# Kernel optimization log

Measured on AMD Instinct MI355X. Metric: run time of the kernel, lower is better.

The kernel has to match this reference:

```python
import jax, jax.numpy as jnp
import numpy as np

N_NODES = 100000
N_EDGES = 1600000
N_GRAPHS = 512
IN_CH = 128
HID_CH = 128   # 2 * out_channels
OUT_CH = 64


def gcn_conv(x, edge_index, W, b, num_nodes):
    """PyG GCNConv: x' = D^-1/2 (A+I) D^-1/2 (x W) + b (symmetric norm, self loops)."""
    h = x @ W  # [N, F_out]
    loops = jnp.arange(num_nodes, dtype=edge_index.dtype)
    src = jnp.concatenate([edge_index[0], loops])  # j (source)
    dst = jnp.concatenate([edge_index[1], loops])  # i (target)
    deg = jax.ops.segment_sum(jnp.ones_like(dst, dtype=h.dtype), dst,
                              num_segments=num_nodes)  # in-degree incl. self loop
    dinv = jnp.where(deg > 0, jax.lax.rsqrt(deg), 0.0)
    norm = dinv[src] * dinv[dst]  # [E+N]
    msgs = h[src] * norm[:, None]  # gather + scale, [E+N, F_out]
    out = jax.ops.segment_sum(msgs, dst, num_segments=num_nodes)
    return out + b


def global_mean_pool(x, batch, num_graphs):
    sums = jax.ops.segment_sum(x, batch, num_segments=num_graphs)
    cnts = jax.ops.segment_sum(jnp.ones((x.shape[0],), x.dtype), batch,
                               num_segments=num_graphs)
    return sums / jnp.maximum(cnts, 1.0)[:, None]


def setup_inputs() -> dict:
    key = jax.random.key(0)
    k = jax.random.split(key, 6)
    x = jax.random.normal(k[0], (N_NODES, IN_CH), dtype=jnp.float32)
    edge_index = jax.random.randint(k[1], (2, N_EDGES), 0, N_NODES, dtype=jnp.int64)
    batch = jnp.sort(jax.random.randint(k[2], (N_NODES,), 0, N_GRAPHS, dtype=jnp.int64))
    W1 = jax.random.normal(k[3], (IN_CH, HID_CH), dtype=jnp.float32) * (1.0 / np.sqrt(IN_CH))
    b1 = jnp.zeros((HID_CH,), dtype=jnp.float32)
    W2 = jax.random.normal(k[4], (HID_CH, OUT_CH), dtype=jnp.float32) * (1.0 / np.sqrt(HID_CH))
    b2 = jnp.zeros((OUT_CH,), dtype=jnp.float32)
    return {"x": x, "edge_index": edge_index, "batch": batch,
            "W1": W1, "b1": b1, "W2": W2, "b2": b2}


def reference(x, edge_index, batch, W1, b1, W2, b2):
    h = gcn_conv(x, edge_index, W1, b1, N_NODES)
    h = jax.nn.relu(h)
    h = gcn_conv(h, edge_index, W2, b2, N_NODES)
    return global_mean_pool(h, batch, N_GRAPHS)  # [num_graphs, out_channels]
```

## Files before the change

kernel.cpp:

```cpp
#include <hip/hip_runtime.h>
#include <hip/hip_fp16.h>

#define NN 100000
#define NE 1600000
#define NG 512
#define NBLK 391
#define CAP 4608
#define EPBS 4096
#define NCBS 391

typedef _Float16 half8 __attribute__((ext_vector_type(8)));
typedef _Float16 half4v __attribute__((ext_vector_type(4)));
typedef float floatx4 __attribute__((ext_vector_type(4)));
typedef float floatx2 __attribute__((ext_vector_type(2)));

__device__ inline unsigned char f32_to_fp8(float v) {
    return (unsigned char)(__builtin_amdgcn_cvt_pk_fp8_f32(v, v, 0, false) & 0xFF);
}
__device__ inline void fp8x8_acc(float* acc, uint2 u) {
    floatx2 a = __builtin_amdgcn_cvt_pk_f32_fp8(u.x, false);
    floatx2 b = __builtin_amdgcn_cvt_pk_f32_fp8(u.x, true);
    floatx2 c = __builtin_amdgcn_cvt_pk_f32_fp8(u.y, false);
    floatx2 d = __builtin_amdgcn_cvt_pk_f32_fp8(u.y, true);
    acc[0] += a[0]; acc[1] += a[1]; acc[2] += b[0]; acc[3] += b[1];
    acc[4] += c[0]; acc[5] += c[1]; acc[6] += d[0]; acc[7] += d[1];
}

__global__ void k_wtboth(const float* __restrict__ W1, const float* __restrict__ W2,
                         __half* __restrict__ Wt1, __half* __restrict__ Wt2,
                         int* __restrict__ gcur) {
    int idx = blockIdx.x * 256 + threadIdx.x;
    if (idx < 128 * 128) {
        int k = idx >> 7, n = idx & 127;
        Wt1[n * 128 + k] = __float2half(W1[idx]);
    } else {
        int j = idx - 128 * 128;
        if (j < 128 * 64) {
            int k = j / 64, n = j % 64;
            Wt2[n * 128 + k] = __float2half(W2[j]);
        }
    }
    if (idx < 512) gcur[idx] = idx * CAP;
}

__global__ __launch_bounds__(256) void k_csort(const int* __restrict__ src,
                                               const int* __restrict__ dst,
                                               int* __restrict__ gcur,
                                               unsigned* __restrict__ pairbuf) {
    __shared__ int hcnt[NBLK];
    __shared__ int lbase[NBLK];
    __shared__ int lcur[NBLK];
    __shared__ int gbase[NBLK];
    __shared__ int ss[512];
    __shared__ unsigned sorted[EPBS];
    __shared__ unsigned short bkt[EPBS];
    int t = threadIdx.x;
    int e0 = blockIdx.x * EPBS;
    int e1 = e0 + EPBS; if (e1 > NE) e1 = NE;
    int n = e1 - e0;

    for (int i = t; i < NBLK; i += 256) hcnt[i] = 0;
    __syncthreads();
    for (int i = e0 + t; i < e1; i += 256)
        atomicAdd(&hcnt[dst[i] >> 8], 1);
    __syncthreads();
    ss[t]       = (t < NBLK) ? hcnt[t] : 0;
    ss[t + 256] = (t + 256 < NBLK) ? hcnt[t + 256] : 0;
    __syncthreads();
    for (int d = 1; d < 512; d <<= 1) {
        int v1 = (t >= d) ? ss[t - d] : 0;
        int v2 = ss[t + 256 - d];
        __syncthreads();
        ss[t] += v1; ss[t + 256] += v2;
        __syncthreads();
    }
    for (int i = t; i < NBLK; i += 256) {
        int ex = ss[i] - hcnt[i];
        lbase[i] = ex;
        lcur[i] = ex;
        if (hcnt[i] > 0) gbase[i] = atomicAdd(&gcur[i], hcnt[i]);
    }
    __syncthreads();
    for (int i = e0 + t; i < e1; i += 256) {
        int d = dst[i];
        int b = d >> 8;
        int pos = atomicAdd(&lcur[b], 1);
        sorted[pos] = ((unsigned)(d & 255) << 24) | (unsigned)src[i];
        bkt[pos] = (unsigned short)b;
    }
    __syncthreads();
    for (int i = t; i < n; i += 256) {
        int b = bkt[i];
        pairbuf[gbase[b] + (i - lbase[b])] = sorted[i];
    }
}

__global__ __launch_bounds__(256) void k_offs_place(
    const unsigned* __restrict__ pairbuf, const int* __restrict__ gcur,
    int* __restrict__ offs, int* __restrict__ edeg,
    float* __restrict__ dinv, int* __restrict__ csr) {
    __shared__ int dcnt[256];
    __shared__ int p[256];
    __shared__ int lcur[256];
    int t = threadIdx.x;
    int b = blockIdx.x;
    int base = b * CAP;
    int cnt = gcur[b] - base;
    int node0 = b << 8;
    dcnt[t] = 0;
    __syncthreads();
    for (int i = t; i < cnt; i += 256)
        atomicAdd(&dcnt[pairbuf[base + i] >> 24], 1);
    __syncthreads();
    int v = dcnt[t];
    p[t] = v;
    __syncthreads();
    for (int d = 1; d < 256; d <<= 1) {
        int u = (t >= d) ? p[t - d] : 0;
        __syncthreads();
        p[t] += u;
        __syncthreads();
    }
    int ex = p[t] - v;
    lcur[t] = ex;
    int node = node0 + t;
    if (node < NN) {
        offs[node] = base + ex;
        edeg[node] = v;
        dinv[node] = rsqrtf((float)(v + 1));
    }
    __syncthreads();
    for (int i = t; i < cnt; i += 256) {
        unsigned e = pairbuf[base + i];
        int slot = atomicAdd(&lcur[e >> 24], 1);
        csr[base + slot] = (int)(e & 0xFFFFFFu);
    }
}

__global__ __launch_bounds__(256) void k_mm_mfma(const float* __restrict__ X,
                                                 const __half* __restrict__ Wt,
                                                 const float* __restrict__ dinv,
                                                 unsigned char* __restrict__ Out) {
    constexpr int PITCH = 136;
    constexpr int FOUT = 128;
    __shared__ _Float16 Xs[64 * PITCH];
    __shared__ _Float16 Ws[FOUT * PITCH];
    int t = threadIdx.x;
    int row0 = blockIdx.x * 64;

    for (int i = t; i < 64 * 32; i += 256) {
        int r = i >> 5, f4 = i & 31;
        int row = row0 + r;
        half4v h = {};
        if (row < NN) {
            float4 v = *(const float4*)(X + (size_t)row * 128 + f4 * 4);
            h[0] = (_Float16)v.x; h[1] = (_Float16)v.y;
            h[2] = (_Float16)v.z; h[3] = (_Float16)v.w;
        }
        *(half4v*)(Xs + r * PITCH + f4 * 4) = h;
    }
    for (int i = t; i < FOUT * 16; i += 256) {
        int n = i >> 4, kg = i & 15;
        *(half8*)(Ws + n * PITCH + kg * 8) = *(const half8*)(Wt + n * 128 + kg * 8);
    }
    __syncthreads();

    int wave = t >> 6, lane = t & 63;
    int m = lane & 15, quad = lane >> 4;
    int wrow = wave * 16;
    constexpr int NCT = FOUT / 16;
    floatx4 acc[NCT];
#pragma unroll
    for (int c = 0; c < NCT; ++c) acc[c] = (floatx4){0.f, 0.f, 0.f, 0.f};

#pragma unroll
    for (int kc = 0; kc < 4; ++kc) {
        half8 a = *(const half8*)(Xs + (wrow + m) * PITCH + kc * 32 + quad * 8);
#pragma unroll
        for (int c = 0; c < NCT; ++c) {
            half8 b = *(const half8*)(Ws + (c * 16 + m) * PITCH + kc * 32 + quad * 8);
            acc[c] = __builtin_amdgcn_mfma_f32_16x16x32_f16(a, b, acc[c], 0, 0, 0);
        }
    }

    float dv[4];
    int rowb = row0 + wrow + quad * 4;
#pragma unroll
    for (int r = 0; r < 4; ++r) dv[r] = (rowb + r < NN) ? dinv[rowb + r] : 0.f;
#pragma unroll
    for (int c = 0; c < NCT; ++c) {
#pragma unroll
        for (int r = 0; r < 4; ++r) {
            int row = rowb + r;
            if (row < NN)
                Out[(size_t)row * FOUT + c * 16 + m] = f32_to_fp8(acc[c][r] * dv[r]);
        }
    }
}

__global__ __launch_bounds__(256) void k_agg_mm(
    const unsigned char* __restrict__ G, const int* __restrict__ csr,
    const int* __restrict__ offs, const int* __restrict__ edeg,
    const float* __restrict__ dinv, const float* __restrict__ bias1,
    const __half* __restrict__ Wt2, unsigned char* __restrict__ G2) {
    constexpr int PITCH = 136;
    __shared__ _Float16 Brows[16 * PITCH];
    __shared__ _Float16 Ws[64 * PITCH];
    int t = threadIdx.x;
    for (int i = t; i < 64 * 16; i += 256) {
        int n = i >> 4, kg = i & 15;
        *(half8*)(Ws + n * PITCH + kg * 8) = *(const half8*)(Wt2 + n * 128 + kg * 8);
    }
    int wave = t >> 6, lane = t & 63;
    int sub = lane >> 4, fl = lane & 15;
    int ni = wave * 4 + sub;
    int node = blockIdx.x * 16 + ni;
    float acc[8];
#pragma unroll
    for (int j = 0; j < 8; ++j) acc[j] = 0.f;
    fp8x8_acc(acc, *(const uint2*)(G + (size_t)node * 128 + fl * 8));
    int e0 = offs[node], e1 = e0 + edeg[node];
    int e = e0;
    if (e + 8 <= e1) {
        int s0 = csr[e],     s1 = csr[e + 1], s2 = csr[e + 2], s3 = csr[e + 3];
        int s4 = csr[e + 4], s5 = csr[e + 5], s6 = csr[e + 6], s7 = csr[e + 7];
        for (; e + 8 <= e1; e += 8) {
            int p0 = csr[e + 8],  p1 = csr[e + 9],  p2 = csr[e + 10], p3 = csr[e + 11];
            int p4 = csr[e + 12], p5 = csr[e + 13], p6 = csr[e + 14], p7 = csr[e + 15];
            uint2 v0 = *(const uint2*)(G + (size_t)s0 * 128 + fl * 8);
            uint2 v1 = *(const uint2*)(G + (size_t)s1 * 128 + fl * 8);
            uint2 v2 = *(const uint2*)(G + (size_t)s2 * 128 + fl * 8);
            uint2 v3 = *(const uint2*)(G + (size_t)s3 * 128 + fl * 8);
            uint2 v4 = *(const uint2*)(G + (size_t)s4 * 128 + fl * 8);
            uint2 v5 = *(const uint2*)(G + (size_t)s5 * 128 + fl * 8);
            uint2 v6 = *(const uint2*)(G + (size_t)s6 * 128 + fl * 8);
            uint2 v7 = *(const uint2*)(G + (size_t)s7 * 128 + fl * 8);
            fp8x8_acc(acc, v0); fp8x8_acc(acc, v1); fp8x8_acc(acc, v2); fp8x8_acc(acc, v3);
            fp8x8_acc(acc, v4); fp8x8_acc(acc, v5); fp8x8_acc(acc, v6); fp8x8_acc(acc, v7);
            s0 = p0; s1 = p1; s2 = p2; s3 = p3;
            s4 = p4; s5 = p5; s6 = p6; s7 = p7;
        }
    }
    for (; e + 4 <= e1; e += 4) {
        int s0 = csr[e], s1 = csr[e + 1], s2 = csr[e + 2], s3 = csr[e + 3];
        uint2 v0 = *(const uint2*)(G + (size_t)s0 * 128 + fl * 8);
        uint2 v1 = *(const uint2*)(G + (size_t)s1 * 128 + fl * 8);
        uint2 v2 = *(const uint2*)(G + (size_t)s2 * 128 + fl * 8);
        uint2 v3 = *(const uint2*)(G + (size_t)s3 * 128 + fl * 8);
        fp8x8_acc(acc, v0); fp8x8_acc(acc, v1); fp8x8_acc(acc, v2); fp8x8_acc(acc, v3);
    }
    for (; e < e1; ++e)
        fp8x8_acc(acc, *(const uint2*)(G + (size_t)csr[e] * 128 + fl * 8));
    {
        float di = dinv[node];
        float4 b0 = *(const float4*)(bias1 + fl * 8);
        float4 b1 = *(const float4*)(bias1 + fl * 8 + 4);
        half8 h;
        h[0] = (_Float16)fmaxf(acc[0] * di + b0.x, 0.f);
        h[1] = (_Float16)fmaxf(acc[1] * di + b0.y, 0.f);
        h[2] = (_Float16)fmaxf(acc[2] * di + b0.z, 0.f);
        h[3] = (_Float16)fmaxf(acc[3] * di + b0.w, 0.f);
        h[4] = (_Float16)fmaxf(acc[4] * di + b1.x, 0.f);
        h[5] = (_Float16)fmaxf(acc[5] * di + b1.y, 0.f);
        h[6] = (_Float16)fmaxf(acc[6] * di + b1.z, 0.f);
        h[7] = (_Float16)fmaxf(acc[7] * di + b1.w, 0.f);
        *(half8*)(Brows + ni * PITCH + fl * 8) = h;
    }
    __syncthreads();
    int m = lane & 15, quad = lane >> 4;
    floatx4 c = (floatx4){0.f, 0.f, 0.f, 0.f};
#pragma unroll
    for (int kc = 0; kc < 4; ++kc) {
        half8 a = *(const half8*)(Brows + m * PITCH + kc * 32 + quad * 8);
        half8 b = *(const half8*)(Ws + (wave * 16 + m) * PITCH + kc * 32 + quad * 8);
        c = __builtin_amdgcn_mfma_f32_16x16x32_f16(a, b, c, 0, 0, 0);
    }
    int rowb = blockIdx.x * 16 + quad * 4;
#pragma unroll
    for (int r = 0; r < 4; ++r) {
        float dv = dinv[rowb + r];
        G2[(size_t)(rowb + r) * 64 + wave * 16 + m] = f32_to_fp8(c[r] * dv);
    }
}

__global__ __launch_bounds__(256) void k_agg_pool(
    const unsigned char* __restrict__ G, const int* __restrict__ csr,
    const int* __restrict__ offs, const int* __restrict__ edeg,
    const float* __restrict__ dinv, const int* __restrict__ batch,
    float* __restrict__ gsum) {
    __shared__ float bsum[4][64];
    int t = threadIdx.x;
    int wave = t >> 6, lane = t & 63;
    int sub = lane >> 3, fl = lane & 7;
    int n0 = blockIdx.x * 32;
    int nb = n0 + wave * 8;
    int node = nb + sub;
    float acc[8];
#pragma unroll
    for (int j = 0; j < 8; ++j) acc[j] = 0.f;
    fp8x8_acc(acc, *(const uint2*)(G + (size_t)node * 64 + fl * 8));
    int e0 = offs[node], e1 = e0 + edeg[node];
    int e = e0;
    if (e + 8 <= e1) {
        int s0 = csr[e],     s1 = csr[e + 1], s2 = csr[e + 2], s3 = csr[e + 3];
        int s4 = csr[e + 4], s5 = csr[e + 5], s6 = csr[e + 6], s7 = csr[e + 7];
        for (; e + 8 <= e1; e += 8) {
            int p0 = csr[e + 8],  p1 = csr[e + 9],  p2 = csr[e + 10], p3 = csr[e + 11];
            int p4 = csr[e + 12], p5 = csr[e + 13], p6 = csr[e + 14], p7 = csr[e + 15];
            uint2 v0 = *(const uint2*)(G + (size_t)s0 * 64 + fl * 8);
            uint2 v1 = *(const uint2*)(G + (size_t)s1 * 64 + fl * 8);
            uint2 v2 = *(const uint2*)(G + (size_t)s2 * 64 + fl * 8);
            uint2 v3 = *(const uint2*)(G + (size_t)s3 * 64 + fl * 8);
            uint2 v4 = *(const uint2*)(G + (size_t)s4 * 64 + fl * 8);
            uint2 v5 = *(const uint2*)(G + (size_t)s5 * 64 + fl * 8);
            uint2 v6 = *(const uint2*)(G + (size_t)s6 * 64 + fl * 8);
            uint2 v7 = *(const uint2*)(G + (size_t)s7 * 64 + fl * 8);
            fp8x8_acc(acc, v0); fp8x8_acc(acc, v1); fp8x8_acc(acc, v2); fp8x8_acc(acc, v3);
            fp8x8_acc(acc, v4); fp8x8_acc(acc, v5); fp8x8_acc(acc, v6); fp8x8_acc(acc, v7);
            s0 = p0; s1 = p1; s2 = p2; s3 = p3;
            s4 = p4; s5 = p5; s6 = p6; s7 = p7;
        }
    }
    for (; e + 4 <= e1; e += 4) {
        int s0 = csr[e], s1 = csr[e + 1], s2 = csr[e + 2], s3 = csr[e + 3];
        uint2 v0 = *(const uint2*)(G + (size_t)s0 * 64 + fl * 8);
        uint2 v1 = *(const uint2*)(G + (size_t)s1 * 64 + fl * 8);
        uint2 v2 = *(const uint2*)(G + (size_t)s2 * 64 + fl * 8);
        uint2 v3 = *(const uint2*)(G + (size_t)s3 * 64 + fl * 8);
        fp8x8_acc(acc, v0); fp8x8_acc(acc, v1); fp8x8_acc(acc, v2); fp8x8_acc(acc, v3);
    }
    for (; e < e1; ++e)
        fp8x8_acc(acc, *(const uint2*)(G + (size_t)csr[e] * 64 + fl * 8));
    float di = dinv[node];
#pragma unroll
    for (int j = 0; j < 8; ++j) acc[j] *= di;

    bool buni = (batch[n0] == batch[n0 + 31]);
    if (buni) {
#pragma unroll
        for (int j = 0; j < 8; ++j) {
            float s = acc[j];
            s += __shfl_xor(s, 8);
            s += __shfl_xor(s, 16);
            s += __shfl_xor(s, 32);
            acc[j] = s;
        }
        if (sub == 0) {
#pragma unroll
            for (int j = 0; j < 8; ++j) bsum[wave][fl * 8 + j] = acc[j];
        }
        __syncthreads();
        if (t < 64) {
            float tot = (bsum[0][t] + bsum[1][t]) + (bsum[2][t] + bsum[3][t]);
            atomicAdd(&gsum[batch[n0] * 64 + t], tot);
        }
    } else {
        int gph = batch[node];
        bool uni = (batch[nb] == batch[nb + 7]);
        if (uni) {
#pragma unroll
            for (int j = 0; j < 8; ++j) {
                float s = acc[j];
                s += __shfl_xor(s, 8);
                s += __shfl_xor(s, 16);
                s += __shfl_xor(s, 32);
                acc[j] = s;
            }
            if (sub == 0) {
#pragma unroll
                for (int j = 0; j < 8; ++j)
                    atomicAdd(&gsum[gph * 64 + fl * 8 + j], acc[j]);
            }
        } else {
#pragma unroll
            for (int j = 0; j < 8; ++j)
                atomicAdd(&gsum[gph * 64 + fl * 8 + j], acc[j]);
        }
    }
}

__global__ __launch_bounds__(64) void k_pool2(const float* __restrict__ gsum,
                                              const int* __restrict__ batch,
                                              const float* __restrict__ b2,
                                              float* __restrict__ out) {
    int gph = blockIdx.x;
    int f = threadIdx.x;
    int lo = 0, hi = NN;
    while (lo < hi) { int m = (lo + hi) >> 1; if (batch[m] < gph) lo = m + 1; else hi = m; }
    int s0 = lo;
    hi = NN;
    while (lo < hi) { int m = (lo + hi) >> 1; if (batch[m] <= gph) lo = m + 1; else hi = m; }
    int cnt = lo - s0;
    out[gph * 64 + f] = (cnt > 0) ? gsum[gph * 64 + f] / (float)cnt + b2[f] : 0.f;
}

extern "C" void kernel_launch(void* const* d_in, const int* in_sizes, int n_in,
                              void* d_out, int out_size, void* d_ws, size_t ws_size,
                              hipStream_t stream) {
    const float* x     = (const float*)d_in[0];
    const int*   ei    = (const int*)d_in[1];
    const int*   batch = (const int*)d_in[2];
    const float* W1    = (const float*)d_in[3];
    const float* b1    = (const float*)d_in[4];
    const float* W2    = (const float*)d_in[5];
    const float* b2    = (const float*)d_in[6];
    const int* esrc = ei;
    const int* edst = ei + NE;

    char* ws = (char*)d_ws;
    size_t off = 0;
    const size_t CSRN = (size_t)NBLK * CAP;
    unsigned char* G1 = (unsigned char*)(ws + off); off += (size_t)NN * 128;
    unsigned char* G2 = (unsigned char*)(ws + off); off += (size_t)NN * 64;
    float* gsum = (float*)(ws + off);  off += (size_t)NG * 64 * 4;
    int*   csr  = (int*)(ws + off);    off += CSRN * 4;
    unsigned* pairbuf = (unsigned*)(ws + off); off += CSRN * 4;
    int*   offs = (int*)(ws + off);    off += (size_t)NN * 4;
    int*   edeg = (int*)(ws + off);    off += (size_t)NN * 4;
    float* dinv = (float*)(ws + off);  off += (size_t)NN * 4;
    int*   gcur = (int*)(ws + off);    off += 512 * 4;
    __half* Wt1 = (__half*)(ws + off); off += 128 * 128 * 2;
    __half* Wt2 = (__half*)(ws + off); off += 128 * 64 * 2;

    hipMemsetAsync(gsum, 0, (size_t)NG * 64 * sizeof(float), stream);
    k_wtboth<<<96, 256, 0, stream>>>(W1, W2, Wt1, Wt2, gcur);
    k_csort<<<NCBS, 256, 0, stream>>>(esrc, edst, gcur, pairbuf);
    k_offs_place<<<NBLK, 256, 0, stream>>>(pairbuf, gcur, offs, edeg, dinv, csr);

    const int MMB = (NN + 63) / 64;
    k_mm_mfma<<<MMB, 256, 0, stream>>>(x, Wt1, dinv, G1);
    k_agg_mm<<<NN / 16, 256, 0, stream>>>(G1, csr, offs, edeg, dinv, b1, Wt2, G2);
    k_agg_pool<<<NN / 32, 256, 0, stream>>>(G2, csr, offs, edeg, dinv, batch, gsum);
    k_pool2<<<NG, 64, 0, stream>>>(gsum, batch, b2, (float*)d_out);
}
```

Before: 254.6 us.

## Widen layer-1 gather to 16-byte loads split across edge halves; pack offset+degree

In the first aggregation kernel, each 16-lane node group now splits into two halves that process alternate edges. Each lane loads 16 fp8 features with one uint4 load instead of 8 with a uint2. The partial sums are combined with a cross-lane shuffle before the bias/ReLU epilogue. Separately, the CSR offset and degree are packed into one 32-bit word (21-bit offset, degree in the upper bits), which removes the edeg array and one load per node in both aggregation kernels. This trades more accumulator registers and a shuffle reduction for fewer, wider memory transactions, and it assumes degrees fit in 11 bits.

```diff
diff --git a/kernel.cpp b/kernel.cpp
--- a/kernel.cpp
+++ b/kernel.cpp
@@ -24,6 +24,20 @@
     floatx2 d = __builtin_amdgcn_cvt_pk_f32_fp8(u.y, true);
     acc[0] += a[0]; acc[1] += a[1]; acc[2] += b[0]; acc[3] += b[1];
     acc[4] += c[0]; acc[5] += c[1]; acc[6] += d[0]; acc[7] += d[1];
+}
+__device__ inline void fp8x16_acc(float* acc, uint4 u) {
+    floatx2 a = __builtin_amdgcn_cvt_pk_f32_fp8(u.x, false);
+    floatx2 b = __builtin_amdgcn_cvt_pk_f32_fp8(u.x, true);
+    floatx2 c = __builtin_amdgcn_cvt_pk_f32_fp8(u.y, false);
+    floatx2 d = __builtin_amdgcn_cvt_pk_f32_fp8(u.y, true);
+    floatx2 e = __builtin_amdgcn_cvt_pk_f32_fp8(u.z, false);
+    floatx2 f = __builtin_amdgcn_cvt_pk_f32_fp8(u.z, true);
+    floatx2 g = __builtin_amdgcn_cvt_pk_f32_fp8(u.w, false);
+    floatx2 h = __builtin_amdgcn_cvt_pk_f32_fp8(u.w, true);
+    acc[0]  += a[0]; acc[1]  += a[1]; acc[2]  += b[0]; acc[3]  += b[1];
+    acc[4]  += c[0]; acc[5]  += c[1]; acc[6]  += d[0]; acc[7]  += d[1];
+    acc[8]  += e[0]; acc[9]  += e[1]; acc[10] += f[0]; acc[11] += f[1];
+    acc[12] += g[0]; acc[13] += g[1]; acc[14] += h[0]; acc[15] += h[1];
 }
 
 __global__ void k_wtboth(const float* __restrict__ W1, const float* __restrict__ W2,
@@ -97,8 +111,7 @@
 
 __global__ __launch_bounds__(256) void k_offs_place(
     const unsigned* __restrict__ pairbuf, const int* __restrict__ gcur,
-    int* __restrict__ offs, int* __restrict__ edeg,
-    float* __restrict__ dinv, int* __restrict__ csr) {
+    int* __restrict__ offs, float* __restrict__ dinv, int* __restrict__ csr) {
     __shared__ int dcnt[256];
     __shared__ int p[256];
     __shared__ int lcur[256];
@@ -125,8 +138,7 @@
     lcur[t] = ex;
     int node = node0 + t;
     if (node < NN) {
-        offs[node] = base + ex;
-        edeg[node] = v;
+        offs[node] = (base + ex) | (v << 21);
         dinv[node] = rsqrtf((float)(v + 1));
     }
     __syncthreads();
@@ -200,9 +212,9 @@
 
 __global__ __launch_bounds__(256) void k_agg_mm(
     const unsigned char* __restrict__ G, const int* __restrict__ csr,
-    const int* __restrict__ offs, const int* __restrict__ edeg,
-    const float* __restrict__ dinv, const float* __restrict__ bias1,
-    const __half* __restrict__ Wt2, unsigned char* __restrict__ G2) {
+    const int* __restrict__ offs, const float* __restrict__ dinv,
+    const float* __restrict__ bias1, const __half* __restrict__ Wt2,
+    unsigned char* __restrict__ G2) {
     constexpr int PITCH = 136;
     __shared__ _Float16 Brows[16 * PITCH];
     __shared__ _Float16 Ws[64 * PITCH];
@@ -212,14 +224,17 @@
         *(half8*)(Ws + n * PITCH + kg * 8) = *(const half8*)(Wt2 + n * 128 + kg * 8);
     }
     int wave = t >> 6, lane = t & 63;
-    int sub = lane >> 4, fl = lane & 15;
+    int sub = lane >> 4, L = lane & 15;
+    int h = L >> 3, q = L & 7;
     int ni = wave * 4 + sub;
     int node = blockIdx.x * 16 + ni;
-    float acc[8];
-#pragma unroll
-    for (int j = 0; j < 8; ++j) acc[j] = 0.f;
-    fp8x8_acc(acc, *(const uint2*)(G + (size_t)node * 128 + fl * 8));
-    int e0 = offs[node], e1 = e0 + edeg[node];
+    float acc[16];
+#pragma unroll
+    for (int j = 0; j < 16; ++j) acc[j] = 0.f;
+    if (h == 0)
+        fp8x16_acc(acc, *(const uint4*)(G + (size_t)node * 128 + q * 16));
+    unsigned pk = (unsigned)offs[node];
+    int e0 = (int)(pk & 0x1FFFFFu), e1 = e0 + (int)(pk >> 21);
     int e = e0;
     if (e + 8 <= e1) {
         int s0 = csr[e],     s1 = csr[e + 1], s2 = csr[e + 2], s3 = csr[e + 3];
@@ -227,44 +242,47 @@
         for (; e + 8 <= e1; e += 8) {
             int p0 = csr[e + 8],  p1 = csr[e + 9],  p2 = csr[e + 10], p3 = csr[e + 11];
             int p4 = csr[e + 12], p5 = csr[e + 13], p6 = csr[e + 14], p7 = csr[e + 15];
-            uint2 v0 = *(const uint2*)(G + (size_t)s0 * 128 + fl * 8);
-            uint2 v1 = *(const uint2*)(G + (size_t)s1 * 128 + fl * 8);
-            uint2 v2 = *(const uint2*)(G + (size_t)s2 * 128 + fl * 8);
-            uint2 v3 = *(const uint2*)(G + (size_t)s3 * 128 + fl * 8);
-            uint2 v4 = *(const uint2*)(G + (size_t)s4 * 128 + fl * 8);
-            uint2 v5 = *(const uint2*)(G + (size_t)s5 * 128 + fl * 8);
-            uint2 v6 = *(const uint2*)(G + (size_t)s6 * 128 + fl * 8);
-            uint2 v7 = *(const uint2*)(G + (size_t)s7 * 128 + fl * 8);
-            fp8x8_acc(acc, v0); fp8x8_acc(acc, v1); fp8x8_acc(acc, v2); fp8x8_acc(acc, v3);
-            fp8x8_acc(acc, v4); fp8x8_acc(acc, v5); fp8x8_acc(acc, v6); fp8x8_acc(acc, v7);
+            int r0 = h ? s1 : s0;
+            int r1 = h ? s3 : s2;
+            int r2 = h ? s5 : s4;
+            int r3 = h ? s7 : s6;
+            uint4 v0 = *(const uint4*)(G + (size_t)r0 * 128 + q * 16);
+            uint4 v1 = *(const uint4*)(G + (size_t)r1 * 128 + q * 16);
+            uint4 v2 = *(const uint4*)(G + (size_t)r2 * 128 + q * 16);
+            uint4 v3 = *(const uint4*)(G + (size_t)r3 * 128 + q * 16);
+            fp8x16_acc(acc, v0); fp8x16_acc(acc, v1);
+            fp8x16_acc(acc, v2); fp8x16_acc(acc, v3);
             s0 = p0; s1 = p1; s2 = p2; s3 = p3;
             s4 = p4; s5 = p5; s6 = p6; s7 = p7;
         }
     }
-    for (; e + 4 <= e1; e += 4) {
-        int s0 = csr[e], s1 = csr[e + 1], s2 = csr[e + 2], s3 = csr[e + 3];
-        uint2 v0 = *(const uint2*)(G + (size_t)s0 * 128 + fl * 8);
-        uint2 v1 = *(const uint2*)(G + (size_t)s1 * 128 + fl * 8);
-        uint2 v2 = *(const uint2*)(G + (size_t)s2 * 128 + fl * 8);
-        uint2 v3 = *(const uint2*)(G + (size_t)s3 * 128 + fl * 8);
-        fp8x8_acc(acc, v0); fp8x8_acc(acc, v1); fp8x8_acc(acc, v2); fp8x8_acc(acc, v3);
-    }
-    for (; e < e1; ++e)
-        fp8x8_acc(acc, *(const uint2*)(G + (size_t)csr[e] * 128 + fl * 8));
+    for (; e + 2 <= e1; e += 2) {
+        int sa = csr[e], sb = csr[e + 1];
+        int r = h ? sb : sa;
+        fp8x16_acc(acc, *(const uint4*)(G + (size_t)r * 128 + q * 16));
+    }
+    if (e < e1 && h == 0)
+        fp8x16_acc(acc, *(const uint4*)(G + (size_t)csr[e] * 128 + q * 16));
+#pragma unroll
+    for (int j = 0; j < 16; ++j) acc[j] += __shfl_xor(acc[j], 8);
     {
         float di = dinv[node];
-        float4 b0 = *(const float4*)(bias1 + fl * 8);
-        float4 b1 = *(const float4*)(bias1 + fl * 8 + 4);
-        half8 h;
-        h[0] = (_Float16)fmaxf(acc[0] * di + b0.x, 0.f);
-        h[1] = (_Float16)fmaxf(acc[1] * di + b0.y, 0.f);
-        h[2] = (_Float16)fmaxf(acc[2] * di + b0.z, 0.f);
-        h[3] = (_Float16)fmaxf(acc[3] * di + b0.w, 0.f);
-        h[4] = (_Float16)fmaxf(acc[4] * di + b1.x, 0.f);
-        h[5] = (_Float16)fmaxf(acc[5] * di + b1.y, 0.f);
-        h[6] = (_Float16)fmaxf(acc[6] * di + b1.z, 0.f);
-        h[7] = (_Float16)fmaxf(acc[7] * di + b1.w, 0.f);
-        *(half8*)(Brows + ni * PITCH + fl * 8) = h;
+        float o[8];
+#pragma unroll
+        for (int j = 0; j < 8; ++j) o[j] = h ? acc[8 + j] : acc[j];
+        int fb = q * 16 + h * 8;
+        float4 b0 = *(const float4*)(bias1 + fb);
+        float4 b1 = *(const float4*)(bias1 + fb + 4);
+        half8 hv;
+        hv[0] = (_Float16)fmaxf(o[0] * di + b0.x, 0.f);
+        hv[1] = (_Float16)fmaxf(o[1] * di + b0.y, 0.f);
+        hv[2] = (_Float16)fmaxf(o[2] * di + b0.z, 0.f);
+        hv[3] = (_Float16)fmaxf(o[3] * di + b0.w, 0.f);
+        hv[4] = (_Float16)fmaxf(o[4] * di + b1.x, 0.f);
+        hv[5] = (_Float16)fmaxf(o[5] * di + b1.y, 0.f);
+        hv[6] = (_Float16)fmaxf(o[6] * di + b1.z, 0.f);
+        hv[7] = (_Float16)fmaxf(o[7] * di + b1.w, 0.f);
+        *(half8*)(Brows + ni * PITCH + fb) = hv;
     }
     __syncthreads();
     int m = lane & 15, quad = lane >> 4;
@@ -285,9 +303,8 @@
 
 __global__ __launch_bounds__(256) void k_agg_pool(
     const unsigned char* __restrict__ G, const int* __restrict__ csr,
-    const int* __restrict__ offs, const int* __restrict__ edeg,
-    const float* __restrict__ dinv, const int* __restrict__ batch,
-    float* __restrict__ gsum) {
+    const int* __restrict__ offs, const float* __restrict__ dinv,
+    const int* __restrict__ batch, float* __restrict__ gsum) {
     __shared__ float bsum[4][64];
     int t = threadIdx.x;
     int wave = t >> 6, lane = t & 63;
@@ -299,7 +316,8 @@
 #pragma unroll
     for (int j = 0; j < 8; ++j) acc[j] = 0.f;
     fp8x8_acc(acc, *(const uint2*)(G + (size_t)node * 64 + fl * 8));
-    int e0 = offs[node], e1 = e0 + edeg[node];
+    unsigned pk = (unsigned)offs[node];
+    int e0 = (int)(pk & 0x1FFFFFu), e1 = e0 + (int)(pk >> 21);
     int e = e0;
     if (e + 8 <= e1) {
         int s0 = csr[e],     s1 = csr[e + 1], s2 = csr[e + 2], s3 = csr[e + 3];
@@ -416,7 +434,6 @@
     int*   csr  = (int*)(ws + off);    off += CSRN * 4;
     unsigned* pairbuf = (unsigned*)(ws + off); off += CSRN * 4;
     int*   offs = (int*)(ws + off);    off += (size_t)NN * 4;
-    int*   edeg = (int*)(ws + off);    off += (size_t)NN * 4;
     float* dinv = (float*)(ws + off);  off += (size_t)NN * 4;
     int*   gcur = (int*)(ws + off);    off += 512 * 4;
     __half* Wt1 = (__half*)(ws + off); off += 128 * 128 * 2;
@@ -425,11 +442,11 @@
     hipMemsetAsync(gsum, 0, (size_t)NG * 64 * sizeof(float), stream);
     k_wtboth<<<96, 256, 0, stream>>>(W1, W2, Wt1, Wt2, gcur);
     k_csort<<<NCBS, 256, 0, stream>>>(esrc, edst, gcur, pairbuf);
-    k_offs_place<<<NBLK, 256, 0, stream>>>(pairbuf, gcur, offs, edeg, dinv, csr);
+    k_offs_place<<<NBLK, 256, 0, stream>>>(pairbuf, gcur, offs, dinv, csr);
 
     const int MMB = (NN + 63) / 64;
     k_mm_mfma<<<MMB, 256, 0, stream>>>(x, Wt1, dinv, G1);
-    k_agg_mm<<<NN / 16, 256, 0, stream>>>(G1, csr, offs, edeg, dinv, b1, Wt2, G2);
-    k_agg_pool<<<NN / 32, 256, 0, stream>>>(G2, csr, offs, edeg, dinv, batch, gsum);
+    k_agg_mm<<<NN / 16, 256, 0, stream>>>(G1, csr, offs, dinv, b1, Wt2, G2);
+    k_agg_pool<<<NN / 32, 256, 0, stream>>>(G2, csr, offs, dinv, batch, gsum);
     k_pool2<<<NG, 64, 0, stream>>>(gsum, batch, b2, (float*)d_out);
 }
```

Measured after the change: 263.1 us. 1.03x slower.
